# Performance work log

Measured on AMD Instinct MI355X. Metric: run time of the kernel, lower is better.

## Reference

```python
import jax, jax.numpy as jnp
import numpy as np

MAX_WORDS = 50257
INPUT_SIZE = 1024
BATCH, SEQ = 8, 2048


def setup_inputs() -> dict:
    key = jax.random.key(0)
    kx, kw, kb = jax.random.split(key, 3)
    x = jax.random.randint(kx, (BATCH, SEQ), 0, MAX_WORDS, dtype=jnp.int64 if jax.config.jax_enable_x64 else jnp.int32)
    # nn.Linear(max_words, input_size): weight [input_size, max_words], bias [input_size]
    W = jax.random.normal(kw, (INPUT_SIZE, MAX_WORDS), dtype=jnp.float32) * 0.02
    b = jax.random.normal(kb, (INPUT_SIZE,), dtype=jnp.float32) * 0.02
    return {"x": x, "W": W, "b": b}


def reference(x, W, b):
    # one_hot(x, V).float() @ W.T + b  ==  gather rows of W.T at x, plus bias.
    # W.T has shape [max_words, input_size]; result [B, S, input_size].
    return jnp.take(W.T, x, axis=0) + b
```

## Files before the change

kernel.cpp:

```cpp
#include <hip/hip_runtime.h>


#define VOCAB 50257
#define DIM   1024
#define NBUCK ((VOCAB + 15) >> 4)
#define NXCD  8
#define TPB   64
#define JSL   128
#define NJS   (DIM / JSL)
#define TSTR  65

__global__ __launch_bounds__(1024) void sort_prep_kernel(
    const int* __restrict__ x, int n, int* __restrict__ offs)
{
    __shared__ int counts[NBUCK];
    __shared__ int wtot[16];
    __shared__ int wbase[16];

    const int tid = threadIdx.x;

    for (int i = tid; i < NBUCK; i += 1024) counts[i] = 0;
    __syncthreads();

    for (int i = tid; i < n; i += 1024)
        atomicAdd(&counts[((unsigned)x[i]) >> 4], 1);
    __syncthreads();

    int c[4];
    const int b0 = tid * 4;
#pragma unroll
    for (int k = 0; k < 4; ++k)
        c[k] = (b0 + k < NBUCK) ? counts[b0 + k] : 0;
    const int partial = c[0] + c[1] + c[2] + c[3];

    const int wave = tid >> 6, lane = tid & 63;
    int s = partial;
    for (int d = 1; d < 64; d <<= 1) {
        int y = __shfl_up(s, d);
        if (lane >= d) s += y;
    }
    if (lane == 63) wtot[wave] = s;
    __syncthreads();
    if (tid < 16) {
        int v = wtot[tid];
        int e = 0;
        for (int w = 0; w < 16; ++w) { if (w == tid) break; e += wtot[w]; }
        (void)v;
        wbase[tid] = e;
    }
    __syncthreads();

    int excl = wbase[wave] + s - partial;
#pragma unroll
    for (int k = 0; k < 4; ++k) {
        if (b0 + k < NBUCK) offs[b0 + k] = excl;
        excl += c[k];
    }
}

__global__ void scatter_kernel(const int* __restrict__ x, int n,
                               int* __restrict__ offs, int* __restrict__ order) {
    int i = blockIdx.x * blockDim.x + threadIdx.x;
    if (i < n) {
        int v = x[i];
        int pos = atomicAdd(&offs[v >> 4], 1);
        order[pos] = (v << 16) | i;
    }
}

__global__ __launch_bounds__(256) void lane_sorted_gather(
    const float* __restrict__ W,
    const float* __restrict__ bias,
    const int* __restrict__ order,
    float* __restrict__ out,
    int n, int q, int r)
{
    extern __shared__ float lds[];
    float* tile = lds;
    int* tTok = (int*)(lds + TPB * TSTR);

    const int bid = blockIdx.x;
    const int xcd = bid & (NXCD - 1);
    const int idx = bid >> 3;
    const int chunk_base = (xcd < r) ? xcd * (q + 1) : r * (q + 1) + (xcd - r) * q;
    const int L = chunk_base + idx;
    const int g  = L >> 3;
    const int js = L & 7;

    const int tid = threadIdx.x;
    const int wave = tid >> 6;
    const int lane = tid & 63;

    const int t0 = g * TPB;
    const int cnt = min(TPB, n - t0);

    const unsigned pk = (unsigned)order[t0 + (lane < cnt ? lane : 0)];
    const int vl = (int)(pk >> 16);
    if (wave == 0) tTok[lane] = (int)(pk & 0xFFFFu);

    const int jb0 = js * JSL;
    const float* __restrict__ Wv = W + vl;
    const int jw = jb0 + wave * 16;
    const int tok = tid >> 2;
    const int qq = tid & 3;

    float a0[8], b0[8];
#pragma unroll
    for (int i = 0; i < 8; ++i) a0[i] = Wv[(size_t)(jw + i) * VOCAB];
#pragma unroll
    for (int i = 0; i < 8; ++i) b0[i] = Wv[(size_t)(jw + 8 + i) * VOCAB];
    __builtin_amdgcn_sched_barrier(0);
#pragma unroll
    for (int i = 0; i < 8; ++i) tile[lane * TSTR + wave * 16 + i] = a0[i];
#pragma unroll
    for (int i = 0; i < 8; ++i) tile[lane * TSTR + wave * 16 + 8 + i] = b0[i];

    float a1[8], b1[8];
#pragma unroll
    for (int i = 0; i < 8; ++i) a1[i] = Wv[(size_t)(jw + 64 + i) * VOCAB];
#pragma unroll
    for (int i = 0; i < 8; ++i) b1[i] = Wv[(size_t)(jw + 72 + i) * VOCAB];
    __builtin_amdgcn_sched_barrier(0);

    __syncthreads();

    const int t_out = (tok < cnt) ? tTok[tok] : -1;
    if (t_out >= 0) {
        float* __restrict__ dst = out + (size_t)t_out * DIM + jb0;
#pragma unroll
        for (int k = 0; k < 4; ++k) {
            const int jloc = k * 16 + qq * 4;
            float4 w4 = *reinterpret_cast<const float4*>(&tile[tok * TSTR + jloc]);
            const float4 b4 = *reinterpret_cast<const float4*>(&bias[jb0 + jloc]);
            w4.x += b4.x; w4.y += b4.y; w4.z += b4.z; w4.w += b4.w;
            *reinterpret_cast<float4*>(dst + jloc) = w4;
        }
    }
    __syncthreads();

#pragma unroll
    for (int i = 0; i < 8; ++i) tile[lane * TSTR + wave * 16 + i] = a1[i];
#pragma unroll
    for (int i = 0; i < 8; ++i) tile[lane * TSTR + wave * 16 + 8 + i] = b1[i];
    __syncthreads();

    if (t_out >= 0) {
        float* __restrict__ dst = out + (size_t)t_out * DIM + jb0 + 64;
#pragma unroll
        for (int k = 0; k < 4; ++k) {
            const int jloc = k * 16 + qq * 4;
            float4 w4 = *reinterpret_cast<const float4*>(&tile[tok * TSTR + jloc]);
            const float4 b4 = *reinterpret_cast<const float4*>(&bias[jb0 + 64 + jloc]);
            w4.x += b4.x; w4.y += b4.y; w4.z += b4.z; w4.w += b4.w;
            *reinterpret_cast<float4*>(dst + jloc) = w4;
        }
    }
}

__global__ __launch_bounds__(256) void gather_direct_kernel(
    const int* __restrict__ x,
    const float* __restrict__ W,
    const float* __restrict__ bias,
    float* __restrict__ out)
{
    const int t = blockIdx.x;
    const int v = x[t];
    const int j0 = threadIdx.x * 4;
    float4 rr;
    rr.x = W[(size_t)(j0 + 0) * VOCAB + v];
    rr.y = W[(size_t)(j0 + 1) * VOCAB + v];
    rr.z = W[(size_t)(j0 + 2) * VOCAB + v];
    rr.w = W[(size_t)(j0 + 3) * VOCAB + v];
    const float4 bb = *reinterpret_cast<const float4*>(bias + j0);
    rr.x += bb.x; rr.y += bb.y; rr.z += bb.z; rr.w += bb.w;
    *reinterpret_cast<float4*>(out + (size_t)t * DIM + j0) = rr;
}

extern "C" void kernel_launch(void* const* d_in, const int* in_sizes, int n_in,
                              void* d_out, int out_size, void* d_ws, size_t ws_size,
                              hipStream_t stream) {
    const int*   x    = (const int*)d_in[0];
    const float* W    = (const float*)d_in[1];
    const float* bias = (const float*)d_in[2];
    float*       out  = (float*)d_out;

    const int n = in_sizes[0];

    const size_t need = (size_t)(NBUCK + n) * sizeof(int);
    if (ws_size < need || n > 65536) {
        gather_direct_kernel<<<n, 256, 0, stream>>>(x, W, bias, out);
        return;
    }

    int* offs   = (int*)d_ws;
    int* order  = offs + NBUCK;

    sort_prep_kernel<<<1, 1024, 0, stream>>>(x, n, offs);
    const int tb = 256;
    scatter_kernel<<<(n + tb - 1) / tb, tb, 0, stream>>>(x, n, offs, order);

    const int ngroups = (n + TPB - 1) / TPB;
    const int nblk = ngroups * NJS;
    const int q = nblk / NXCD, r = nblk % NXCD;
    const size_t lds_bytes = (TPB * TSTR) * sizeof(float) + TPB * sizeof(int);
    lane_sorted_gather<<<nblk, 256, lds_bytes, stream>>>(W, bias, order, out, n, q, r);
}
```

Before: 60.00 us.

## Vectorize histogram loads, restructure gather chunks, use nontemporal output stores

The histogram pass now reads token ids as int4 vectors with a scalar tail loop, and the wave-base prefix loop is simplified. The gather kernel becomes a loop over two 64-column chunks that loads, stages and writes each chunk in turn. Before, all 32 loads per thread were issued before the first barrier; now the second chunk's loads wait until after the first chunk is written, which lowers register pressure but reduces loads in flight. Output stores become nontemporal to avoid polluting cache with write-once data.

```diff
diff --git a/kernel.cpp b/kernel.cpp
--- a/kernel.cpp
+++ b/kernel.cpp
@@ -10,6 +10,8 @@
 #define NJS   (DIM / JSL)
 #define TSTR  65
 
+typedef float f32x4 __attribute__((ext_vector_type(4)));
+
 __global__ __launch_bounds__(1024) void sort_prep_kernel(
     const int* __restrict__ x, int n, int* __restrict__ offs)
 {
@@ -22,7 +24,16 @@
     for (int i = tid; i < NBUCK; i += 1024) counts[i] = 0;
     __syncthreads();
 
-    for (int i = tid; i < n; i += 1024)
+    const int n4 = n >> 2;
+    const int4* __restrict__ x4 = (const int4*)x;
+    for (int i = tid; i < n4; i += 1024) {
+        const int4 v = x4[i];
+        atomicAdd(&counts[((unsigned)v.x) >> 4], 1);
+        atomicAdd(&counts[((unsigned)v.y) >> 4], 1);
+        atomicAdd(&counts[((unsigned)v.z) >> 4], 1);
+        atomicAdd(&counts[((unsigned)v.w) >> 4], 1);
+    }
+    for (int i = (n4 << 2) + tid; i < n; i += 1024)
         atomicAdd(&counts[((unsigned)x[i]) >> 4], 1);
     __syncthreads();
 
@@ -42,10 +53,8 @@
     if (lane == 63) wtot[wave] = s;
     __syncthreads();
     if (tid < 16) {
-        int v = wtot[tid];
         int e = 0;
-        for (int w = 0; w < 16; ++w) { if (w == tid) break; e += wtot[w]; }
-        (void)v;
+        for (int w = 0; w < tid; ++w) e += wtot[w];
         wbase[tid] = e;
     }
     __syncthreads();
@@ -100,60 +109,48 @@
 
     const int jb0 = js * JSL;
     const float* __restrict__ Wv = W + vl;
-    const int jw = jb0 + wave * 16;
     const int tok = tid >> 2;
     const int qq = tid & 3;
 
-    float a0[8], b0[8];
-#pragma unroll
-    for (int i = 0; i < 8; ++i) a0[i] = Wv[(size_t)(jw + i) * VOCAB];
-#pragma unroll
-    for (int i = 0; i < 8; ++i) b0[i] = Wv[(size_t)(jw + 8 + i) * VOCAB];
-    __builtin_amdgcn_sched_barrier(0);
-#pragma unroll
-    for (int i = 0; i < 8; ++i) tile[lane * TSTR + wave * 16 + i] = a0[i];
-#pragma unroll
-    for (int i = 0; i < 8; ++i) tile[lane * TSTR + wave * 16 + 8 + i] = b0[i];
-
-    float a1[8], b1[8];
-#pragma unroll
-    for (int i = 0; i < 8; ++i) a1[i] = Wv[(size_t)(jw + 64 + i) * VOCAB];
-#pragma unroll
-    for (int i = 0; i < 8; ++i) b1[i] = Wv[(size_t)(jw + 72 + i) * VOCAB];
-    __builtin_amdgcn_sched_barrier(0);
-
-    __syncthreads();
-
-    const int t_out = (tok < cnt) ? tTok[tok] : -1;
-    if (t_out >= 0) {
-        float* __restrict__ dst = out + (size_t)t_out * DIM + jb0;
-#pragma unroll
-        for (int k = 0; k < 4; ++k) {
-            const int jloc = k * 16 + qq * 4;
-            float4 w4 = *reinterpret_cast<const float4*>(&tile[tok * TSTR + jloc]);
-            const float4 b4 = *reinterpret_cast<const float4*>(&bias[jb0 + jloc]);
-            w4.x += b4.x; w4.y += b4.y; w4.z += b4.z; w4.w += b4.w;
-            *reinterpret_cast<float4*>(dst + jloc) = w4;
+#pragma unroll
+    for (int ch = 0; ch < JSL / 64; ++ch) {
+        const int jb = jb0 + ch * 64 + wave * 16;
+
+        float a[8];
+#pragma unroll
+        for (int i = 0; i < 8; ++i)
+            a[i] = Wv[(size_t)(jb + i) * VOCAB];
+        __builtin_amdgcn_sched_barrier(0);
+#pragma unroll
+        for (int i = 0; i < 8; ++i)
+            tile[lane * TSTR + wave * 16 + i] = a[i];
+
+        float b[8];
+#pragma unroll
+        for (int i = 0; i < 8; ++i)
+            b[i] = Wv[(size_t)(jb + 8 + i) * VOCAB];
+        __builtin_amdgcn_sched_barrier(0);
+#pragma unroll
+        for (int i = 0; i < 8; ++i)
+            tile[lane * TSTR + wave * 16 + 8 + i] = b[i];
+
+        __syncthreads();
+
+        if (tok < cnt) {
+            const int t = tTok[tok];
+            float* __restrict__ dst = out + (size_t)t * DIM + jb0 + ch * 64;
+#pragma unroll
+            for (int k = 0; k < 4; ++k) {
+                const int jloc = k * 16 + qq * 4;
+                const float4 w4 = *reinterpret_cast<const float4*>(&tile[tok * TSTR + jloc]);
+                const float4 b4 = *reinterpret_cast<const float4*>(&bias[jb0 + ch * 64 + jloc]);
+                f32x4 o;
+                o.x = w4.x + b4.x; o.y = w4.y + b4.y;
+                o.z = w4.z + b4.z; o.w = w4.w + b4.w;
+                __builtin_nontemporal_store(o, reinterpret_cast<f32x4*>(dst + jloc));
+            }
         }
-    }
-    __syncthreads();
-
-#pragma unroll
-    for (int i = 0; i < 8; ++i) tile[lane * TSTR + wave * 16 + i] = a1[i];
-#pragma unroll
-    for (int i = 0; i < 8; ++i) tile[lane * TSTR + wave * 16 + 8 + i] = b1[i];
-    __syncthreads();
-
-    if (t_out >= 0) {
-        float* __restrict__ dst = out + (size_t)t_out * DIM + jb0 + 64;
-#pragma unroll
-        for (int k = 0; k < 4; ++k) {
-            const int jloc = k * 16 + qq * 4;
-            float4 w4 = *reinterpret_cast<const float4*>(&tile[tok * TSTR + jloc]);
-            const float4 b4 = *reinterpret_cast<const float4*>(&bias[jb0 + 64 + jloc]);
-            w4.x += b4.x; w4.y += b4.y; w4.z += b4.z; w4.w += b4.w;
-            *reinterpret_cast<float4*>(dst + jloc) = w4;
-        }
+        __syncthreads();
     }
 }
 
```

Result: faster. 56.14 us (-6.4%).
